# Performance work log

Measured on AMD Instinct MI355X. Metric: run time of the kernel, lower is better.

The kernel has to match this reference:

```python
import jax, jax.numpy as jnp
import numpy as np

H = 1024       # hidden_size
VOCAB = 32000  # output_size
L = 128        # max_length
B = 64         # batch


def setup_inputs() -> dict:
    key = jax.random.key(0)
    ks = jax.random.split(key, 16)
    inp = {
        "input_ids": jax.random.randint(ks[0], (1, B), 0, VOCAB),
        "hidden": jax.random.normal(ks[1], (1, B, H), jnp.float32),
        "encoder_outputs": jax.random.normal(ks[2], (L, B, H), jnp.float32),
        # parameters
        "emb": jax.random.normal(ks[3], (VOCAB, H), jnp.float32) * 0.02,
        "attn_W": jax.random.normal(ks[4], (H, 2 * H), jnp.float32) * 0.02,
        "attn_b": jnp.zeros((H,), jnp.float32),
        "v": jax.random.uniform(ks[5], (H,), jnp.float32),
        "w_ih": jax.random.normal(ks[6], (3 * H, 2 * H), jnp.float32) * 0.02,
        "w_hh": jax.random.normal(ks[7], (3 * H, H), jnp.float32) * 0.02,
        "b_ih": jnp.zeros((3 * H,), jnp.float32),
        "b_hh": jnp.zeros((3 * H,), jnp.float32),
        "out_W": jax.random.normal(ks[8], (VOCAB, 3 * H), jnp.float32) * 0.02,
        "out_b": jnp.zeros((VOCAB,), jnp.float32),
    }
    return inp


def reference(input_ids, hidden, encoder_outputs, emb, attn_W, attn_b, v,
              w_ih, w_hh, b_ih, b_hh, out_W, out_b):
    # Dropout in eval mode (identity).
    embedded = emb[input_ids]                      # [1, B, H]
    eo = jnp.transpose(encoder_outputs, (1, 0, 2))  # [B, L, H]
    h0 = hidden[0]                                  # [B, H]

    # Additive (Bahdanau) attention score
    h_rep = jnp.broadcast_to(h0[:, None, :], (eo.shape[0], eo.shape[1], h0.shape[-1]))
    cat = jnp.concatenate([eo, h_rep], axis=-1)     # [B, L, 2H]
    energy = jnp.tanh(jnp.einsum('blk,hk->blh', cat, attn_W) + attn_b)  # [B, L, H]
    scores = jnp.einsum('blh,h->bl', energy, v)     # [B, L]
    attention = jax.nn.softmax(scores, axis=-1)     # [B, L]
    weighted = jnp.einsum('bl,blh->bh', attention, eo)  # [B, H]

    # GRU cell (single layer, single timestep), PyTorch gate order r,z,n
    x = jnp.concatenate([embedded[0], weighted], axis=-1)  # [B, 2H]
    gx = x @ w_ih.T + b_ih                                  # [B, 3H]
    gh = h0 @ w_hh.T + b_hh                                 # [B, 3H]
    xr, xz, xn = jnp.split(gx, 3, axis=-1)
    hr, hz, hn = jnp.split(gh, 3, axis=-1)
    r = jax.nn.sigmoid(xr + hr)
    z = jax.nn.sigmoid(xz + hz)
    n = jnp.tanh(xn + r * hn)
    h_new = (1.0 - z) * n + z * h0                          # [B, H]

    out_cat = jnp.concatenate([h_new, weighted, embedded[0]], axis=-1)  # [B, 3H]
    output = out_cat @ out_W.T + out_b                      # [B, VOCAB]
    return output, h_new[None], attention[:, None, :]
```

## Files before the change

### kernel.cpp

```cpp
#include <hip/hip_runtime.h>
#include <math.h>

#define Hdim 1024
#define VOC 32000
#define LSEQ 128
#define BSZ 64

typedef __attribute__((ext_vector_type(8))) short bf16x8;
typedef __attribute__((ext_vector_type(4))) float f32x4;

__device__ __forceinline__ float fast_tanhf(float x) {
    return 1.0f - 2.0f / (__expf(2.0f * x) + 1.0f);
}
__device__ __forceinline__ float sigmoidf(float x) {
    return 1.0f / (1.0f + __expf(-x));
}
__device__ __forceinline__ short f2bf(float f) {
    unsigned u = __float_as_uint(f);
    unsigned r = (u + 0x7fffu + ((u >> 16) & 1u)) >> 16;
    return (short)r;
}

__device__ __forceinline__ void gl_lds16(const short* g, short* l) {
    __builtin_amdgcn_global_load_lds(
        (const __attribute__((address_space(1))) unsigned*)g,
        (__attribute__((address_space(3))) unsigned*)l, 16, 0, 0);
}

__device__ __forceinline__ void stage16(const float* __restrict__ src, short* dst) {
    f32x4 v0 = *(const f32x4*)(src);
    f32x4 v1 = *(const f32x4*)(src + 4);
    f32x4 v2 = *(const f32x4*)(src + 8);
    f32x4 v3 = *(const f32x4*)(src + 12);
    bf16x8 p0, p1;
    p0[0] = f2bf(v0[0]); p0[1] = f2bf(v0[1]); p0[2] = f2bf(v0[2]); p0[3] = f2bf(v0[3]);
    p0[4] = f2bf(v1[0]); p0[5] = f2bf(v1[1]); p0[6] = f2bf(v1[2]); p0[7] = f2bf(v1[3]);
    p1[0] = f2bf(v2[0]); p1[1] = f2bf(v2[1]); p1[2] = f2bf(v2[2]); p1[3] = f2bf(v2[3]);
    p1[4] = f2bf(v3[0]); p1[5] = f2bf(v3[1]); p1[6] = f2bf(v3[2]); p1[7] = f2bf(v3[3]);
    *(bf16x8*)(dst) = p0;
    *(bf16x8*)(dst + 8) = p1;
}

__global__ __launch_bounds__(256) void conv_ug(
    const float* __restrict__ enc, const float* __restrict__ attnW,
    const float* __restrict__ hidden, const float* __restrict__ emb,
    const int* __restrict__ ids,
    short* __restrict__ enc_bf, short* __restrict__ attnW1_bf,
    short* __restrict__ hidden_bf, short* __restrict__ x_bf,
    float* __restrict__ u4)
{
    __shared__ short As[64 * 72];
    __shared__ short Bs[128 * 72];

    if (blockIdx.x < 1024) {
        const int NG_ENC = 1048576, NG_AW = 131072, NG_H = 8192, NG_EMB = 8192;
        const int total = NG_ENC + NG_AW + NG_H + NG_EMB;
        for (int g = blockIdx.x * 256 + threadIdx.x; g < total; g += 1024 * 256) {
            const float* src; short* dst;
            if (g < NG_ENC) {
                src = enc + (size_t)g * 8; dst = enc_bf + (size_t)g * 8;
            } else if (g < NG_ENC + NG_AW) {
                const int i = g - NG_ENC, h = i >> 7, c = i & 127;
                src = attnW + (size_t)h * 2048 + c * 8;
                dst = attnW1_bf + (size_t)h * 1024 + c * 8;
            } else if (g < NG_ENC + NG_AW + NG_H) {
                const int i = g - NG_ENC - NG_AW;
                src = hidden + (size_t)i * 8; dst = hidden_bf + (size_t)i * 8;
            } else {
                const int i = g - NG_ENC - NG_AW - NG_H, b = i >> 7, c = i & 127;
                src = emb + (size_t)ids[b] * Hdim + c * 8;
                dst = x_bf + (size_t)b * 2048 + c * 8;
            }
            f32x4 a = *(const f32x4*)(src);
            f32x4 b = *(const f32x4*)(src + 4);
            bf16x8 p;
            p[0] = f2bf(a[0]); p[1] = f2bf(a[1]); p[2] = f2bf(a[2]); p[3] = f2bf(a[3]);
            p[4] = f2bf(b[0]); p[5] = f2bf(b[1]); p[6] = f2bf(b[2]); p[7] = f2bf(b[3]);
            *(bf16x8*)(dst) = p;
        }
        return;
    }

    const int id = blockIdx.x - 1024;
    const int n0 = (id & 7) * 128;
    const int kstart = (id >> 3) * 256;
    float* Cp = u4 + (size_t)(id >> 3) * (BSZ * Hdim);

    const int t = threadIdx.x;
    const int lane = t & 63, wave = t >> 6;
    const int lr = lane & 15, kh = lane >> 4;
    const int ar = t >> 2, ac = (t & 3) * 16;
    const int br = t >> 1, bc = (t & 1) * 32;

    f32x4 acc[4][2] = {};

    for (int k0 = 0; k0 < 256; k0 += 64) {
        const int kg = kstart + k0;
        stage16(hidden + (size_t)ar * Hdim + kg + ac, As + ar * 72 + ac);
        stage16(attnW + (size_t)(n0 + br) * 2048 + 1024 + kg + bc,      Bs + br * 72 + bc);
        stage16(attnW + (size_t)(n0 + br) * 2048 + 1024 + kg + bc + 16, Bs + br * 72 + bc + 16);
        __syncthreads();
#pragma unroll
        for (int kk = 0; kk < 64; kk += 32) {
            bf16x8 af[4], bfr[2];
#pragma unroll
            for (int mi = 0; mi < 4; ++mi)
                af[mi] = *(const bf16x8*)(As + (mi * 16 + lr) * 72 + kk + kh * 8);
#pragma unroll
            for (int ni = 0; ni < 2; ++ni)
                bfr[ni] = *(const bf16x8*)(Bs + (wave * 32 + ni * 16 + lr) * 72 + kk + kh * 8);
#pragma unroll
            for (int mi = 0; mi < 4; ++mi)
#pragma unroll
                for (int ni = 0; ni < 2; ++ni)
                    acc[mi][ni] = __builtin_amdgcn_mfma_f32_16x16x32_bf16(
                        af[mi], bfr[ni], acc[mi][ni], 0, 0, 0);
        }
        __syncthreads();
    }

#pragma unroll
    for (int mi = 0; mi < 4; ++mi)
#pragma unroll
        for (int ni = 0; ni < 2; ++ni) {
            const int col = n0 + wave * 32 + ni * 16 + lr;
#pragma unroll
            for (int r = 0; r < 4; ++r)
                Cp[(size_t)(mi * 16 + kh * 4 + r) * Hdim + col] = acc[mi][ni][r];
        }
}

__device__ __forceinline__ void sgemm_body(
    char* smem,
    const short* __restrict__ A, int lda,
    const float* __restrict__ B, int ldb,
    const float* __restrict__ bias,
    float* __restrict__ C, int ldc,
    int n0, int kstart, int klen, bool rmw)
{
    short* As = (short*)smem;
    short* Bs = (short*)(smem + 18432);

    const int t = threadIdx.x;
    const int lane = t & 63, wave = t >> 6;
    const int wm = wave >> 2, wn = wave & 3;
    const int lr = lane & 15, kh = lane >> 4;

    const int sr = t >> 3, sc = (t & 7) * 8;
    const short* Ap = A + (size_t)sr * lda + kstart + sc;
    const float* Bp = B + (size_t)(n0 + sr) * ldb + kstart + sc;

    const int nkt = klen >> 6;

    bf16x8 pa = *(const bf16x8*)(Ap);
    f32x4 pb0 = *(const f32x4*)(Bp);
    f32x4 pb1 = *(const f32x4*)(Bp + 4);
    *(bf16x8*)(&As[sr * 72 + sc]) = pa;
    {
        bf16x8 q;
        q[0] = f2bf(pb0[0]); q[1] = f2bf(pb0[1]); q[2] = f2bf(pb0[2]); q[3] = f2bf(pb0[3]);
        q[4] = f2bf(pb1[0]); q[5] = f2bf(pb1[1]); q[6] = f2bf(pb1[2]); q[7] = f2bf(pb1[3]);
        *(bf16x8*)(&Bs[sr * 72 + sc]) = q;
    }

    f32x4 acc[2] = {};

    for (int kt = 0; kt < nkt; ++kt) {
        const int co = (kt & 1) * 4608;
        if (kt + 1 < nkt) {
            const int kn = (kt + 1) * 64;
            pa  = *(const bf16x8*)(Ap + kn);
            pb0 = *(const f32x4*)(Bp + kn);
            pb1 = *(const f32x4*)(Bp + kn + 4);
        }
        __syncthreads();
#pragma unroll
        for (int kk = 0; kk < 64; kk += 32) {
            bf16x8 af0 = *(const bf16x8*)(&As[co + (wm * 32 + lr) * 72 + kk + kh * 8]);
            bf16x8 af1 = *(const bf16x8*)(&As[co + (wm * 32 + 16 + lr) * 72 + kk + kh * 8]);
            bf16x8 bfr = *(const bf16x8*)(&Bs[co + (wn * 16 + lr) * 72 + kk + kh * 8]);
            acc[0] = __builtin_amdgcn_mfma_f32_16x16x32_bf16(af0, bfr, acc[0], 0, 0, 0);
            acc[1] = __builtin_amdgcn_mfma_f32_16x16x32_bf16(af1, bfr, acc[1], 0, 0, 0);
        }
        if (kt + 1 < nkt) {
            const int no = ((kt + 1) & 1) * 4608;
            *(bf16x8*)(&As[no + sr * 72 + sc]) = pa;
            bf16x8 q;
            q[0] = f2bf(pb0[0]); q[1] = f2bf(pb0[1]); q[2] = f2bf(pb0[2]); q[3] = f2bf(pb0[3]);
            q[4] = f2bf(pb1[0]); q[5] = f2bf(pb1[1]); q[6] = f2bf(pb1[2]); q[7] = f2bf(pb1[3]);
            *(bf16x8*)(&Bs[no + sr * 72 + sc]) = q;
        }
    }

    const int col = n0 + wn * 16 + lr;
    const float bb = bias ? bias[col] : 0.0f;
#pragma unroll
    for (int mi = 0; mi < 2; ++mi)
#pragma unroll
        for (int r = 0; r < 4; ++r) {
            const size_t idx = (size_t)(wm * 32 + mi * 16 + kh * 4 + r) * ldc + col;
            const float prev = rmw ? C[idx] : 0.0f;
            C[idx] = prev + acc[mi][r] + bb;
        }
}

__device__ __forceinline__ void attn_body(
    char* smem,
    const short* __restrict__ enc_bf, const short* __restrict__ W1_bf,
    const float* __restrict__ u4, const float* __restrict__ attnb,
    const float* __restrict__ vvec, float* __restrict__ scores_part,
    int aid)
{
    short* As = (short*)smem;
    short* Bs = (short*)(smem + 16384);
    float* red = (float*)(smem + 32768);

    const int t = threadIdx.x;
    const int lane = t & 63, wave = t >> 6;
    const int wr = wave >> 2, wc = wave & 3;
    const int lr = lane & 15, kh = lane >> 4;
    const int m0 = (aid & 63) * 128;
    const int n0 = (aid >> 6) * 128;

    const int o1 = t * 16;
    const int o2 = 8192 + t * 16;
    const int r1 = o1 >> 7, c1 = (o1 & 127) >> 1;
    const int r2 = o2 >> 7, c2 = (o2 & 127) >> 1;

    f32x4 acc[4][2] = {};

    for (int kg = 0; kg < Hdim; kg += 64) {
        gl_lds16(enc_bf + (size_t)(m0 + r1) * Hdim + kg + c1, As + (o1 >> 1));
        gl_lds16(enc_bf + (size_t)(m0 + r2) * Hdim + kg + c2, As + (o2 >> 1));
        gl_lds16(W1_bf + (size_t)(n0 + r1) * Hdim + kg + c1, Bs + (o1 >> 1));
        gl_lds16(W1_bf + (size_t)(n0 + r2) * Hdim + kg + c2, Bs + (o2 >> 1));
        __syncthreads();
#pragma unroll
        for (int kk = 0; kk < 64; kk += 32) {
            bf16x8 af[4], bfr[2];
#pragma unroll
            for (int mi = 0; mi < 4; ++mi)
                af[mi] = *(const bf16x8*)(As + (wr * 64 + mi * 16 + lr) * 64 + kk + kh * 8);
#pragma unroll
            for (int ni = 0; ni < 2; ++ni)
                bfr[ni] = *(const bf16x8*)(Bs + (wc * 32 + ni * 16 + lr) * 64 + kk + kh * 8);
#pragma unroll
            for (int mi = 0; mi < 4; ++mi)
#pragma unroll
                for (int ni = 0; ni < 2; ++ni)
                    acc[mi][ni] = __builtin_amdgcn_mfma_f32_16x16x32_bf16(
                        af[mi], bfr[ni], acc[mi][ni], 0, 0, 0);
        }
        __syncthreads();
    }

    float* u_lds = (float*)smem;
    for (int i = t; i < 64 * 128; i += 512) {
        const int b = i >> 7, hl = i & 127;
        const size_t g = (size_t)b * Hdim + n0 + hl;
        u_lds[i] = u4[g] + u4[65536 + g] + u4[2 * 65536 + g] + u4[3 * 65536 + g]
                 + attnb[n0 + hl];
    }
    __syncthreads();

    float sv[16];
#pragma unroll
    for (int mi = 0; mi < 4; ++mi)
#pragma unroll
        for (int r = 0; r < 4; ++r) {
            const int b = mi * 16 + kh * 4 + r;
            float s = 0.0f;
#pragma unroll
            for (int ni = 0; ni < 2; ++ni) {
                const int hl = wc * 32 + ni * 16 + lr;
                const float e = fast_tanhf(acc[mi][ni][r] + u_lds[b * 128 + hl]);
                s += e * vvec[n0 + hl];
            }
            sv[mi * 4 + r] = s;
        }
#pragma unroll
    for (int i = 0; i < 16; ++i) {
#pragma unroll
        for (int d = 1; d < 16; d <<= 1)
            sv[i] += __shfl_xor(sv[i], d, 64);
    }
    if (lr == 0) {
#pragma unroll
        for (int mi = 0; mi < 4; ++mi)
#pragma unroll
            for (int r = 0; r < 4; ++r)
                red[wave * 64 + mi * 16 + kh * 4 + r] = sv[mi * 4 + r];
    }
    __syncthreads();
    if (t < 128) {
        const int wrr = t >> 6, lrow = t & 63;
        scores_part[(size_t)(aid >> 6) * (LSEQ * BSZ) + m0 + t] =
            red[(wrr * 4 + 0) * 64 + lrow] + red[(wrr * 4 + 1) * 64 + lrow] +
            red[(wrr * 4 + 2) * 64 + lrow] + red[(wrr * 4 + 3) * 64 + lrow];
    }
}

__global__ __launch_bounds__(512) void attn_oproj(
    const short* __restrict__ enc_bf, const short* __restrict__ W1_bf,
    const float* __restrict__ u4, const float* __restrict__ attnb,
    const float* __restrict__ vvec, float* __restrict__ scores_part,
    const short* __restrict__ x_bf, const float* __restrict__ out_W,
    const float* __restrict__ out_b, float* __restrict__ logits)
{
    __shared__ __align__(16) char smem[36864];
    const int i = blockIdx.x;
    const int s = i >> 3, r = i & 7;
    if ((s & 1) == 0) {
        const int aid = (s >> 1) * 8 + r;
        attn_body(smem, enc_bf, W1_bf, u4, attnb, vvec, scores_part, aid);
    } else {
        const int gid = (s >> 1) * 8 + r;
        if (gid < 500)
            sgemm_body(smem, x_bf, 2048, out_W + 2048, 3072, out_b,
                       logits, VOC, gid * 64, 0, 1024, false);
    }
}

__global__ __launch_bounds__(128) void softmax_weighted(
    const float* __restrict__ sp,
    const short* __restrict__ enc_bf,
    float* __restrict__ attn_out,
    short* __restrict__ x_bf,
    short* __restrict__ hw_bf)
{
    const int b = blockIdx.x, hg = blockIdx.y, t = threadIdx.x;
    __shared__ float aw[LSEQ];
    __shared__ float red[LSEQ];

    float s = 0.0f;
#pragma unroll
    for (int g = 0; g < 8; ++g) s += sp[g * (LSEQ * BSZ) + t * 64 + b];
    red[t] = s;
    __syncthreads();
    for (int off = 64; off > 0; off >>= 1) {
        if (t < off) red[t] = fmaxf(red[t], red[t + off]);
        __syncthreads();
    }
    const float mx = red[0];
    __syncthreads();
    const float e = __expf(s - mx);
    red[t] = e;
    __syncthreads();
    for (int off = 64; off > 0; off >>= 1) {
        if (t < off) red[t] += red[t + off];
        __syncthreads();
    }
    const float p = e / red[0];
    aw[t] = p;
    if (hg == 0) attn_out[(size_t)b * LSEQ + t] = p;
    __syncthreads();

    const int h = hg * 256 + t * 2;
    float a0 = 0.0f, a1 = 0.0f;
#pragma unroll 8
    for (int l = 0; l < LSEQ; ++l) {
        const unsigned w = *(const unsigned*)(enc_bf + ((size_t)l * BSZ + b) * Hdim + h);
        const float pw = aw[l];
        a0 = fmaf(pw, __uint_as_float(w << 16), a0);
        a1 = fmaf(pw, __uint_as_float(w & 0xffff0000u), a1);
    }
    const unsigned packed = (unsigned)(unsigned short)f2bf(a0)
                          | ((unsigned)(unsigned short)f2bf(a1) << 16);
    *(unsigned*)(x_bf + (size_t)b * 2048 + 1024 + h) = packed;
    *(unsigned*)(hw_bf + (size_t)b * 2048 + 1024 + h) = packed;
}

__global__ __launch_bounds__(512) void gxgh_stream(
    const short* __restrict__ x_bf, const float* __restrict__ w_ih,
    const short* __restrict__ hidden_bf, const float* __restrict__ w_hh,
    float* __restrict__ gx4, float* __restrict__ gh4)
{
    __shared__ __align__(16) char smem[36864];
    const size_t P = (size_t)BSZ * 3 * Hdim;
    if (blockIdx.x < 48)
        sgemm_body(smem, x_bf, 2 * Hdim, w_ih, 2 * Hdim, nullptr,
                   gx4 + blockIdx.y * P, 3 * Hdim,
                   blockIdx.x * 64, blockIdx.y * 512, 512, false);
    else
        sgemm_body(smem, hidden_bf, Hdim, w_hh, Hdim, nullptr,
                   gh4 + blockIdx.y * P, 3 * Hdim,
                   (blockIdx.x - 48) * 64, blockIdx.y * 256, 256, false);
}

__global__ __launch_bounds__(256) void gru_kernel(
    const float* __restrict__ gx4, const float* __restrict__ gh4,
    const float* __restrict__ b_ih, const float* __restrict__ b_hh,
    const float* __restrict__ h0,
    float* __restrict__ hnew_out, short* __restrict__ hw_bf)
{
    const int idx = blockIdx.x * 256 + threadIdx.x;
    const int b = idx >> 10, h = idx & 1023;
    const size_t g3 = (size_t)b * (3 * Hdim);
    const size_t P = (size_t)BSZ * 3 * Hdim;
    float xr = b_ih[h], xz = b_ih[Hdim + h], xn = b_ih[2 * Hdim + h];
    float hr = b_hh[h], hz = b_hh[Hdim + h], hn = b_hh[2 * Hdim + h];
#pragma unroll
    for (int s = 0; s < 4; ++s) {
        xr += gx4[s * P + g3 + h];
        xz += gx4[s * P + g3 + Hdim + h];
        xn += gx4[s * P + g3 + 2 * Hdim + h];
        hr += gh4[s * P + g3 + h];
        hz += gh4[s * P + g3 + Hdim + h];
        hn += gh4[s * P + g3 + 2 * Hdim + h];
    }
    const float r = sigmoidf(xr + hr);
    const float z = sigmoidf(xz + hz);
    const float n = fast_tanhf(xn + r * hn);
    const float hv = (1.0f - z) * n + z * h0[(size_t)b * Hdim + h];
    hnew_out[(size_t)b * Hdim + h] = hv;
    hw_bf[(size_t)b * 2048 + h] = f2bf(hv);
}

__global__ __launch_bounds__(512) void oproj_hw(
    const short* __restrict__ hw_bf, const float* __restrict__ out_W,
    float* __restrict__ logits)
{
    __shared__ __align__(16) char smem[36864];
    sgemm_body(smem, hw_bf, 2048, out_W, 3072, nullptr,
               logits, VOC, blockIdx.x * 64, 0, 2048, true);
}

extern "C" void kernel_launch(void* const* d_in, const int* in_sizes, int n_in,
                              void* d_out, int out_size, void* d_ws, size_t ws_size,
                              hipStream_t stream)
{
    const int*   ids    = (const int*)d_in[0];
    const float* hidden = (const float*)d_in[1];
    const float* enc    = (const float*)d_in[2];
    const float* emb    = (const float*)d_in[3];
    const float* attnW  = (const float*)d_in[4];
    const float* attnb  = (const float*)d_in[5];
    const float* vvec   = (const float*)d_in[6];
    const float* w_ih   = (const float*)d_in[7];
    const float* w_hh   = (const float*)d_in[8];
    const float* b_ih   = (const float*)d_in[9];
    const float* b_hh   = (const float*)d_in[10];
    const float* out_W  = (const float*)d_in[11];
    const float* out_b  = (const float*)d_in[12];

    float* out        = (float*)d_out;
    float* out_logits = out;
    float* out_hnew   = out + (size_t)BSZ * VOC;
    float* out_attn   = out_hnew + (size_t)BSZ * Hdim;

    float* ws = (float*)d_ws;
    short* enc_bf    = (short*)ws;
    short* attnW1_bf = (short*)(ws + 4194304);
    short* hidden_bf = (short*)(ws + 4718592);
    float* ws_u4     = ws + 4751360;
    float* ws_sp     = ws_u4 + 262144;
    short* x_bf      = (short*)(ws_sp + 65536);
    short* hw_bf     = (short*)(ws_sp + 131072);
    float* ws_gx4    = ws_sp + 196608;
    float* ws_gh4    = ws_gx4 + 786432;

    conv_ug<<<dim3(1056), 256, 0, stream>>>(
        enc, attnW, hidden, emb, ids,
        enc_bf, attnW1_bf, hidden_bf, x_bf, ws_u4);

    attn_oproj<<<dim3(1016), 512, 0, stream>>>(
        enc_bf, attnW1_bf, ws_u4, attnb, vvec, ws_sp,
        x_bf, out_W, out_b, out_logits);

    softmax_weighted<<<dim3(BSZ, 4), 128, 0, stream>>>(
        ws_sp, enc_bf, out_attn, x_bf, hw_bf);

    gxgh_stream<<<dim3(96, 4), 512, 0, stream>>>(
        x_bf, w_ih, hidden_bf, w_hh, ws_gx4, ws_gh4);

    gru_kernel<<<dim3(BSZ * Hdim / 256), 256, 0, stream>>>(
        ws_gx4, ws_gh4, b_ih, b_hh, hidden, out_hnew, hw_bf);

    oproj_hw<<<dim3(VOC / 64), 512, 0, stream>>>(
        hw_bf, out_W, out_logits);
}
```

Before: 171.2 us.

## Move weighted-context output projection into the GRU-gate GEMM kernel; unroll sgemm pipeline

```diff
diff --git a/kernel.cpp b/kernel.cpp
--- a/kernel.cpp
+++ b/kernel.cpp
@@ -19,6 +19,12 @@
     unsigned u = __float_as_uint(f);
     unsigned r = (u + 0x7fffu + ((u >> 16) & 1u)) >> 16;
     return (short)r;
+}
+__device__ __forceinline__ bf16x8 packbf(f32x4 a, f32x4 b) {
+    bf16x8 q;
+    q[0] = f2bf(a[0]); q[1] = f2bf(a[1]); q[2] = f2bf(a[2]); q[3] = f2bf(a[3]);
+    q[4] = f2bf(b[0]); q[5] = f2bf(b[1]); q[6] = f2bf(b[2]); q[7] = f2bf(b[3]);
+    return q;
 }
 
 __device__ __forceinline__ void gl_lds16(const short* g, short* l) {
@@ -32,13 +38,8 @@
     f32x4 v1 = *(const f32x4*)(src + 4);
     f32x4 v2 = *(const f32x4*)(src + 8);
     f32x4 v3 = *(const f32x4*)(src + 12);
-    bf16x8 p0, p1;
-    p0[0] = f2bf(v0[0]); p0[1] = f2bf(v0[1]); p0[2] = f2bf(v0[2]); p0[3] = f2bf(v0[3]);
-    p0[4] = f2bf(v1[0]); p0[5] = f2bf(v1[1]); p0[6] = f2bf(v1[2]); p0[7] = f2bf(v1[3]);
-    p1[0] = f2bf(v2[0]); p1[1] = f2bf(v2[1]); p1[2] = f2bf(v2[2]); p1[3] = f2bf(v2[3]);
-    p1[4] = f2bf(v3[0]); p1[5] = f2bf(v3[1]); p1[6] = f2bf(v3[2]); p1[7] = f2bf(v3[3]);
-    *(bf16x8*)(dst) = p0;
-    *(bf16x8*)(dst + 8) = p1;
+    *(bf16x8*)(dst)     = packbf(v0, v1);
+    *(bf16x8*)(dst + 8) = packbf(v2, v3);
 }
 
 __global__ __launch_bounds__(256) void conv_ug(
@@ -73,10 +74,7 @@
             }
             f32x4 a = *(const f32x4*)(src);
             f32x4 b = *(const f32x4*)(src + 4);
-            bf16x8 p;
-            p[0] = f2bf(a[0]); p[1] = f2bf(a[1]); p[2] = f2bf(a[2]); p[3] = f2bf(a[3]);
-            p[4] = f2bf(b[0]); p[5] = f2bf(b[1]); p[6] = f2bf(b[2]); p[7] = f2bf(b[3]);
-            *(bf16x8*)(dst) = p;
+            *(bf16x8*)(dst) = packbf(a, b);
         }
         return;
     }
@@ -152,43 +150,54 @@
 
     const int nkt = klen >> 6;
 
-    bf16x8 pa = *(const bf16x8*)(Ap);
-    f32x4 pb0 = *(const f32x4*)(Bp);
-    f32x4 pb1 = *(const f32x4*)(Bp + 4);
-    *(bf16x8*)(&As[sr * 72 + sc]) = pa;
-    {
-        bf16x8 q;
-        q[0] = f2bf(pb0[0]); q[1] = f2bf(pb0[1]); q[2] = f2bf(pb0[2]); q[3] = f2bf(pb0[3]);
-        q[4] = f2bf(pb1[0]); q[5] = f2bf(pb1[1]); q[6] = f2bf(pb1[2]); q[7] = f2bf(pb1[3]);
-        *(bf16x8*)(&Bs[sr * 72 + sc]) = q;
-    }
+    bf16x8 paE = *(const bf16x8*)(Ap);
+    f32x4 pb0E = *(const f32x4*)(Bp);
+    f32x4 pb1E = *(const f32x4*)(Bp + 4);
+    *(bf16x8*)(&As[sr * 72 + sc]) = paE;
+    *(bf16x8*)(&Bs[sr * 72 + sc]) = packbf(pb0E, pb1E);
+    bf16x8 paO = *(const bf16x8*)(Ap + 64);
+    f32x4 pb0O = *(const f32x4*)(Bp + 64);
+    f32x4 pb1O = *(const f32x4*)(Bp + 68);
 
     f32x4 acc[2] = {};
 
-    for (int kt = 0; kt < nkt; ++kt) {
-        const int co = (kt & 1) * 4608;
-        if (kt + 1 < nkt) {
-            const int kn = (kt + 1) * 64;
-            pa  = *(const bf16x8*)(Ap + kn);
-            pb0 = *(const f32x4*)(Bp + kn);
-            pb1 = *(const f32x4*)(Bp + kn + 4);
-        }
-        __syncthreads();
+    for (int kt = 0; kt < nkt; kt += 2) {
+        __syncthreads();
+        if (kt + 2 < nkt) {
+            const int kn = (kt + 2) * 64;
+            paE  = *(const bf16x8*)(Ap + kn);
+            pb0E = *(const f32x4*)(Bp + kn);
+            pb1E = *(const f32x4*)(Bp + kn + 4);
+        }
 #pragma unroll
         for (int kk = 0; kk < 64; kk += 32) {
-            bf16x8 af0 = *(const bf16x8*)(&As[co + (wm * 32 + lr) * 72 + kk + kh * 8]);
-            bf16x8 af1 = *(const bf16x8*)(&As[co + (wm * 32 + 16 + lr) * 72 + kk + kh * 8]);
-            bf16x8 bfr = *(const bf16x8*)(&Bs[co + (wn * 16 + lr) * 72 + kk + kh * 8]);
+            bf16x8 af0 = *(const bf16x8*)(&As[(wm * 32 + lr) * 72 + kk + kh * 8]);
+            bf16x8 af1 = *(const bf16x8*)(&As[(wm * 32 + 16 + lr) * 72 + kk + kh * 8]);
+            bf16x8 bfr = *(const bf16x8*)(&Bs[(wn * 16 + lr) * 72 + kk + kh * 8]);
             acc[0] = __builtin_amdgcn_mfma_f32_16x16x32_bf16(af0, bfr, acc[0], 0, 0, 0);
             acc[1] = __builtin_amdgcn_mfma_f32_16x16x32_bf16(af1, bfr, acc[1], 0, 0, 0);
         }
-        if (kt + 1 < nkt) {
-            const int no = ((kt + 1) & 1) * 4608;
-            *(bf16x8*)(&As[no + sr * 72 + sc]) = pa;
-            bf16x8 q;
-            q[0] = f2bf(pb0[0]); q[1] = f2bf(pb0[1]); q[2] = f2bf(pb0[2]); q[3] = f2bf(pb0[3]);
-            q[4] = f2bf(pb1[0]); q[5] = f2bf(pb1[1]); q[6] = f2bf(pb1[2]); q[7] = f2bf(pb1[3]);
-            *(bf16x8*)(&Bs[no + sr * 72 + sc]) = q;
+        *(bf16x8*)(&As[4608 + sr * 72 + sc]) = paO;
+        *(bf16x8*)(&Bs[4608 + sr * 72 + sc]) = packbf(pb0O, pb1O);
+
+        __syncthreads();
+        if (kt + 3 < nkt) {
+            const int kn = (kt + 3) * 64;
+            paO  = *(const bf16x8*)(Ap + kn);
+            pb0O = *(const f32x4*)(Bp + kn);
+            pb1O = *(const f32x4*)(Bp + kn + 4);
+        }
+#pragma unroll
+        for (int kk = 0; kk < 64; kk += 32) {
+            bf16x8 af0 = *(const bf16x8*)(&As[4608 + (wm * 32 + lr) * 72 + kk + kh * 8]);
+            bf16x8 af1 = *(const bf16x8*)(&As[4608 + (wm * 32 + 16 + lr) * 72 + kk + kh * 8]);
+            bf16x8 bfr = *(const bf16x8*)(&Bs[4608 + (wn * 16 + lr) * 72 + kk + kh * 8]);
+            acc[0] = __builtin_amdgcn_mfma_f32_16x16x32_bf16(af0, bfr, acc[0], 0, 0, 0);
+            acc[1] = __builtin_amdgcn_mfma_f32_16x16x32_bf16(af1, bfr, acc[1], 0, 0, 0);
+        }
+        if (kt + 2 < nkt) {
+            *(bf16x8*)(&As[sr * 72 + sc]) = paE;
+            *(bf16x8*)(&Bs[sr * 72 + sc]) = packbf(pb0E, pb1E);
         }
     }
 
@@ -325,8 +334,7 @@
     const float* __restrict__ sp,
     const short* __restrict__ enc_bf,
     float* __restrict__ attn_out,
-    short* __restrict__ x_bf,
-    short* __restrict__ hw_bf)
+    short* __restrict__ x_bf)
 {
     const int b = blockIdx.x, hg = blockIdx.y, t = threadIdx.x;
     __shared__ float aw[LSEQ];
@@ -367,31 +375,42 @@
     const unsigned packed = (unsigned)(unsigned short)f2bf(a0)
                           | ((unsigned)(unsigned short)f2bf(a1) << 16);
     *(unsigned*)(x_bf + (size_t)b * 2048 + 1024 + h) = packed;
-    *(unsigned*)(hw_bf + (size_t)b * 2048 + 1024 + h) = packed;
-}
-
-__global__ __launch_bounds__(512) void gxgh_stream(
+}
+
+__global__ __launch_bounds__(512) void gxghw(
     const short* __restrict__ x_bf, const float* __restrict__ w_ih,
     const short* __restrict__ hidden_bf, const float* __restrict__ w_hh,
+    const float* __restrict__ out_W, float* __restrict__ logits,
     float* __restrict__ gx4, float* __restrict__ gh4)
 {
     __shared__ __align__(16) char smem[36864];
+    const int i = blockIdx.x;
+    const int s = i >> 3, r = i & 7;
     const size_t P = (size_t)BSZ * 3 * Hdim;
-    if (blockIdx.x < 48)
-        sgemm_body(smem, x_bf, 2 * Hdim, w_ih, 2 * Hdim, nullptr,
-                   gx4 + blockIdx.y * P, 3 * Hdim,
-                   blockIdx.x * 64, blockIdx.y * 512, 512, false);
-    else
-        sgemm_body(smem, hidden_bf, Hdim, w_hh, Hdim, nullptr,
-                   gh4 + blockIdx.y * P, 3 * Hdim,
-                   (blockIdx.x - 48) * 64, blockIdx.y * 256, 256, false);
+    if (s < 96 && (s & 1) == 0) {
+        const int gid = (s >> 1) * 8 + r;
+        const int bx = gid % 96, by = gid / 96;
+        if (bx < 48)
+            sgemm_body(smem, x_bf, 2048, w_ih, 2048, nullptr,
+                       gx4 + by * P, 3072, bx * 64, by * 512, 512, false);
+        else
+            sgemm_body(smem, hidden_bf, 1024, w_hh, 1024, nullptr,
+                       gh4 + by * P, 3072, (bx - 48) * 64, by * 256, 256, false);
+    } else {
+        int wid;
+        if (s < 96) wid = (s >> 1) * 8 + r;
+        else        wid = 384 + (s - 96) * 8 + r;
+        if (wid < 500)
+            sgemm_body(smem, x_bf + 1024, 2048, out_W + 1024, 3072, nullptr,
+                       logits, VOC, wid * 64, 0, 1024, true);
+    }
 }
 
 __global__ __launch_bounds__(256) void gru_kernel(
     const float* __restrict__ gx4, const float* __restrict__ gh4,
     const float* __restrict__ b_ih, const float* __restrict__ b_hh,
     const float* __restrict__ h0,
-    float* __restrict__ hnew_out, short* __restrict__ hw_bf)
+    float* __restrict__ hnew_out, short* __restrict__ h_bf)
 {
     const int idx = blockIdx.x * 256 + threadIdx.x;
     const int b = idx >> 10, h = idx & 1023;
@@ -413,16 +432,16 @@
     const float n = fast_tanhf(xn + r * hn);
     const float hv = (1.0f - z) * n + z * h0[(size_t)b * Hdim + h];
     hnew_out[(size_t)b * Hdim + h] = hv;
-    hw_bf[(size_t)b * 2048 + h] = f2bf(hv);
-}
-
-__global__ __launch_bounds__(512) void oproj_hw(
-    const short* __restrict__ hw_bf, const float* __restrict__ out_W,
+    h_bf[(size_t)b * 1024 + h] = f2bf(hv);
+}
+
+__global__ __launch_bounds__(512) void oproj_h(
+    const short* __restrict__ h_bf, const float* __restrict__ out_W,
     float* __restrict__ logits)
 {
     __shared__ __align__(16) char smem[36864];
-    sgemm_body(smem, hw_bf, 2048, out_W, 3072, nullptr,
-               logits, VOC, blockIdx.x * 64, 0, 2048, true);
+    sgemm_body(smem, h_bf, 1024, out_W, 3072, nullptr,
+               logits, VOC, blockIdx.x * 64, 0, 1024, true);
 }
 
 extern "C" void kernel_launch(void* const* d_in, const int* in_sizes, int n_in,
@@ -455,8 +474,8 @@
     float* ws_u4     = ws + 4751360;
     float* ws_sp     = ws_u4 + 262144;
     short* x_bf      = (short*)(ws_sp + 65536);
-    short* hw_bf     = (short*)(ws_sp + 131072);
-    float* ws_gx4    = ws_sp + 196608;
+    short* h_bf      = (short*)(ws_sp + 131072);
+    float* ws_gx4    = ws_sp + 163840;
     float* ws_gh4    = ws_gx4 + 786432;
 
     conv_ug<<<dim3(1056), 256, 0, stream>>>(
@@ -468,14 +487,14 @@
         x_bf, out_W, out_b, out_logits);
 
     softmax_weighted<<<dim3(BSZ, 4), 128, 0, stream>>>(
-        ws_sp, enc_bf, out_attn, x_bf, hw_bf);
-
-    gxgh_stream<<<dim3(96, 4), 512, 0, stream>>>(
-        x_bf, w_ih, hidden_bf, w_hh, ws_gx4, ws_gh4);
+        ws_sp, enc_bf, out_attn, x_bf);
+
+    gxghw<<<dim3(888), 512, 0, stream>>>(
+        x_bf, w_ih, hidden_bf, w_hh, out_W, out_logits, ws_gx4, ws_gh4);
 
     gru_kernel<<<dim3(BSZ * Hdim / 256), 256, 0, stream>>>(
-        ws_gx4, ws_gh4, b_ih, b_hh, hidden, out_hnew, hw_bf);
-
-    oproj_hw<<<dim3(VOC / 64), 512, 0, stream>>>(
-        hw_bf, out_W, out_logits);
-}
+        ws_gx4, ws_gh4, b_ih, b_hh, hidden, out_hnew, h_bf);
+
+    oproj_h<<<dim3(VOC / 64), 512, 0, stream>>>(
+        h_bf, out_W, out_logits);
+}
```

Result: slower. 185.7 us (+8.4%).
